# Optimization experiments

Hardware: AMD Instinct MI355X
Metric: run time of the kernel (lower is better)

The kernel has to match this reference:

```python
import jax, jax.numpy as jnp
import numpy as np

DROPOUT = 0.1  # module init kwarg


def setup_inputs() -> dict:
    key = jax.random.key(0)
    k_w, k_m, k_i = jax.random.split(key, 3)
    V, D = 50257, 1024
    B, S = 8, 2048
    weight = jax.random.normal(k_w, (V, D), dtype=jnp.float32)
    # uniform draws used to form the per-row bernoulli keep mask (V, 1)
    mask_u = jax.random.uniform(k_m, (V, 1), dtype=jnp.float32)
    words = jax.random.randint(k_i, (B, S), 0, V, dtype=jnp.int64)
    return {"weight": weight, "mask_u": mask_u, "words": words}


def reference(weight, mask_u, words):
    keep = 1.0 - DROPOUT
    # row-wise bernoulli mask, kept rows scaled by 1/keep (inverted dropout)
    mask = (mask_u < keep).astype(weight.dtype) / keep          # (V, 1)
    masked_weight = mask * weight                                # (V, D)
    # F.embedding with padding_idx=-1 (none), no max_norm -> plain gather
    return masked_weight[words]                                  # (B, S, D)
```

## Files before the change

### kernel.cpp

```cpp
#include <hip/hip_runtime.h>
#include <hip/hip_bf16.h>


__global__ __launch_bounds__(256) void embed_dropout_kernel(
    const float* __restrict__ weight,
    const float* __restrict__ mask_u,
    const int* __restrict__ words,
    float* __restrict__ out,
    int D,
    int n_tokens)
{
    const int row = blockIdx.x;
    if (row >= n_tokens) return;

    const int idx = words[row];
    const float keep = 0.9f;
    const float scale = (mask_u[idx] < keep) ? (1.0f / keep) : 0.0f;

    const float4* __restrict__ src =
        reinterpret_cast<const float4*>(weight + (size_t)idx * (size_t)D);
    float4* __restrict__ dst =
        reinterpret_cast<float4*>(out + (size_t)row * (size_t)D);

    const int nvec = D >> 2;
    for (int i = threadIdx.x; i < nvec; i += blockDim.x) {
        float4 v = src[i];
        v.x *= scale; v.y *= scale; v.z *= scale; v.w *= scale;
        dst[i] = v;
    }
}

extern "C" void kernel_launch(void* const* d_in, const int* in_sizes, int n_in,
                              void* d_out, int out_size, void* d_ws, size_t ws_size,
                              hipStream_t stream) {
    const float* weight = (const float*)d_in[0];
    const float* mask_u = (const float*)d_in[1];
    const int*   words  = (const int*)d_in[2];
    float* out = (float*)d_out;

    const int V = in_sizes[1];
    const int D = in_sizes[0] / V;
    const int n_tokens = in_sizes[2];
    (void)out_size; (void)d_ws; (void)ws_size; (void)n_in;

    dim3 grid(n_tokens);
    dim3 block(256);
    embed_dropout_kernel<<<grid, block, 0, stream>>>(
        weight, mask_u, words, out, D, n_tokens);
}
```

Before: 26.00 us.

## Process eight rows per block with batched loads and nontemporal stores

Adds a kernel specialized for D=1024 where each 256-thread block gathers eight token rows, issuing all eight row loads before scaling and storing them. Output writes use nontemporal stores to avoid polluting the cache with streaming data. The goal is more memory-level parallelism per thread and less cache thrash; the cost is eight times fewer blocks and more registers per thread. A generic fallback is kept for other widths.

```diff
diff --git a/kernel.cpp b/kernel.cpp
--- a/kernel.cpp
+++ b/kernel.cpp
@@ -2,31 +2,65 @@
 #include <hip/hip_bf16.h>
 
 
-__global__ __launch_bounds__(256) void embed_dropout_kernel(
+using f32x4 = __attribute__((ext_vector_type(4))) float;
+
+constexpr int RPB = 8;
+
+__global__ __launch_bounds__(256) void embed_dropout_1024(
     const float* __restrict__ weight,
     const float* __restrict__ mask_u,
     const int* __restrict__ words,
     float* __restrict__ out,
-    int D,
     int n_tokens)
+{
+    constexpr int D = 1024;
+    const int row0 = blockIdx.x * RPB;
+    const int t = threadIdx.x;
+
+    int   idx[RPB];
+    float scl[RPB];
+#pragma unroll
+    for (int r = 0; r < RPB; ++r) {
+        const int row = row0 + r;
+        idx[r] = (row < n_tokens) ? words[row] : 0;
+        scl[r] = (mask_u[idx[r]] < 0.9f) ? (1.0f / 0.9f) : 0.0f;
+    }
+
+    f32x4 v[RPB];
+#pragma unroll
+    for (int r = 0; r < RPB; ++r) {
+        const f32x4* src =
+            reinterpret_cast<const f32x4*>(weight + (size_t)idx[r] * D);
+        v[r] = src[t];
+    }
+
+#pragma unroll
+    for (int r = 0; r < RPB; ++r) {
+        const int row = row0 + r;
+        if (row < n_tokens) {
+            f32x4 w = v[r] * scl[r];
+            f32x4* dst = reinterpret_cast<f32x4*>(out + (size_t)row * D);
+            __builtin_nontemporal_store(w, &dst[t]);
+        }
+    }
+}
+
+__global__ __launch_bounds__(256) void embed_dropout_generic(
+    const float* __restrict__ weight,
+    const float* __restrict__ mask_u,
+    const int* __restrict__ words,
+    float* __restrict__ out,
+    int D, int n_tokens)
 {
     const int row = blockIdx.x;
     if (row >= n_tokens) return;
-
     const int idx = words[row];
-    const float keep = 0.9f;
-    const float scale = (mask_u[idx] < keep) ? (1.0f / keep) : 0.0f;
-
-    const float4* __restrict__ src =
-        reinterpret_cast<const float4*>(weight + (size_t)idx * (size_t)D);
-    float4* __restrict__ dst =
-        reinterpret_cast<float4*>(out + (size_t)row * (size_t)D);
-
-    const int nvec = D >> 2;
-    for (int i = threadIdx.x; i < nvec; i += blockDim.x) {
-        float4 v = src[i];
-        v.x *= scale; v.y *= scale; v.z *= scale; v.w *= scale;
-        dst[i] = v;
+    const float scale = (mask_u[idx] < 0.9f) ? (1.0f / 0.9f) : 0.0f;
+    const f32x4* src = reinterpret_cast<const f32x4*>(weight + (size_t)idx * (size_t)D);
+    f32x4* dst = reinterpret_cast<f32x4*>(out + (size_t)row * (size_t)D);
+    for (int i = threadIdx.x; i < (D >> 2); i += blockDim.x) {
+        f32x4 v = src[i] * scale;
+        __builtin_nontemporal_store(v, &dst[i]);
     }
 }
 
@@ -43,8 +77,12 @@
     const int n_tokens = in_sizes[2];
     (void)out_size; (void)d_ws; (void)ws_size; (void)n_in;
 
-    dim3 grid(n_tokens);
-    dim3 block(256);
-    embed_dropout_kernel<<<grid, block, 0, stream>>>(
-        weight, mask_u, words, out, D, n_tokens);
+    if (D == 1024) {
+        dim3 grid((n_tokens + RPB - 1) / RPB);
+        embed_dropout_1024<<<grid, dim3(256), 0, stream>>>(
+            weight, mask_u, words, out, n_tokens);
+    } else {
+        embed_dropout_generic<<<dim3(n_tokens), dim3(256), 0, stream>>>(
+            weight, mask_u, words, out, D, n_tokens);
+    }
 }
```

After: 26.18 us. Within noise of the previous version (+0.7%).
